# Kernel tuning notes

Hardware: AMD Instinct MI355X
Metric: run time of the kernel (lower is better)

## Reference

```python
import jax, jax.numpy as jnp
import numpy as np

B, T, N_EMBED, HEAD_SIZE = 512, 256, 384, 64

def setup_inputs() -> dict:
    key = jax.random.key(0)
    k1, k2, k3, k4 = jax.random.split(key, 4)
    x = jax.random.normal(k1, (B, T, N_EMBED), dtype=jnp.float32)
    # nn.Linear(n_embed, head_size, bias=False) weights, stored as [in, out] for x @ W
    scale = 1.0 / np.sqrt(N_EMBED)
    Wk = jax.random.uniform(k2, (N_EMBED, HEAD_SIZE), jnp.float32, -scale, scale)
    Wq = jax.random.uniform(k3, (N_EMBED, HEAD_SIZE), jnp.float32, -scale, scale)
    Wv = jax.random.uniform(k4, (N_EMBED, HEAD_SIZE), jnp.float32, -scale, scale)
    return {"x": x, "Wk": Wk, "Wq": Wq, "Wv": Wv}

def reference(x, Wk, Wq, Wv):
    # Single causal self-attention head (dropout in eval mode / identity)
    k = x @ Wk  # [B, T, H]
    q = x @ Wq
    v = x @ Wv
    wei = jnp.einsum('bth,bsh->bts', q, k) * (HEAD_SIZE ** -0.5)  # [B, T, T]
    causal = jnp.tril(jnp.ones((T, T), dtype=bool))
    wei = jnp.where(causal, wei, -jnp.inf)
    wei = jax.nn.softmax(wei, axis=-1)
    out = jnp.einsum('bts,bsh->bth', wei, v)  # [B, T, H]
    return out
```

## Files before the change

### kernel.cpp

```cpp
#include <hip/hip_runtime.h>
#include <stdint.h>


typedef short s16x8 __attribute__((ext_vector_type(8)));
typedef short s16x4 __attribute__((ext_vector_type(4)));
typedef float f32x4 __attribute__((ext_vector_type(4)));

#define LOG2E_OVER_8 0.18033688011112042f

__device__ inline short f2bf(float f) {
  union { float f; uint32_t u; } v; v.f = f;
  uint32_t r = (v.u + 0x7fffu + ((v.u >> 16) & 1u)) >> 16;
  return (short)r;
}

__global__ __launch_bounds__(256) void prep_w(const float* __restrict__ Wk,
                                              const float* __restrict__ Wq,
                                              const float* __restrict__ Wv,
                                              short* __restrict__ Wt3) {
  int idx = blockIdx.x * 256 + threadIdx.x;
  int j = idx & 7;
  int lane = (idx >> 3) & 63;
  int rest = idx >> 9;
  int ntile = rest % 12;
  int kc = rest / 12;
  int n = ntile * 16 + (lane & 15);
  int kk = (lane >> 4) * 8 + j;
  int col = n & 63;
  int w = n >> 6;
  const float* W = (w == 0) ? Wk : (w == 1) ? Wq : Wv;
  float v = W[(kc * 32 + kk) * 64 + col];
  if (w == 1) v *= LOG2E_OVER_8;
  Wt3[idx] = f2bf(v);
}

__global__ __launch_bounds__(1024) void fused_head(const float* __restrict__ x,
                                                   const short* __restrict__ Wt3,
                                                   float* __restrict__ out) {
  __shared__ __align__(16) short LDS[81920];
  short* Kf = LDS;
  short* Qf = LDS + 16384;
  short* Vf = LDS + 32768;
  short* Pb = LDS + 49152;
  short* Xc = LDS + 49152;
  short* Wsl = LDS + 49152 + 8192;

  const int tid = threadIdx.x;
  const int wave = tid >> 6;
  const int lane = tid & 63;
  const int l15 = lane & 15;
  const int quad = lane >> 4;
  const int b = blockIdx.x;
  const float* xb = x + (long)b * (256 * 384);

  const int mgrp = wave >> 2;
  const int ngrp = wave & 3;

  const int m0s = tid >> 3;
  const int kq0 = (tid & 7) * 4;
  const int xoff0 = m0s * 384 + kq0;
  const int xoff1 = xoff0 + 128 * 384;
  const int lds0 = (m0s >> 4) * 512 + ((m0s & 15) + (kq0 >> 3) * 16) * 8 + (kq0 & 7);
  const int lds1 = lds0 + 8 * 512;
  const bool wact = (tid < 768);

  f32x4 acc[4][3];
#pragma unroll
  for (int i = 0; i < 4; ++i)
#pragma unroll
    for (int k2 = 0; k2 < 3; ++k2) acc[i][k2] = (f32x4)0.0f;

  f32x4 xa0 = *(const f32x4*)(xb + xoff0);
  f32x4 xa1 = *(const f32x4*)(xb + xoff1);
  s16x8 wv;
  if (wact) wv = *(const s16x8*)(Wt3 + tid * 8);

  for (int kc = 0; kc < 12; ++kc) {
    __syncthreads();
    s16x4 h0, h1;
    h0[0] = f2bf(xa0[0]); h0[1] = f2bf(xa0[1]); h0[2] = f2bf(xa0[2]); h0[3] = f2bf(xa0[3]);
    h1[0] = f2bf(xa1[0]); h1[1] = f2bf(xa1[1]); h1[2] = f2bf(xa1[2]); h1[3] = f2bf(xa1[3]);
    *(s16x4*)(Xc + lds0) = h0;
    *(s16x4*)(Xc + lds1) = h1;
    if (wact) *(s16x8*)(Wsl + tid * 8) = wv;
    __syncthreads();
    if (kc < 11) {
      xa0 = *(const f32x4*)(xb + xoff0 + (kc + 1) * 32);
      xa1 = *(const f32x4*)(xb + xoff1 + (kc + 1) * 32);
      if (wact) wv = *(const s16x8*)(Wt3 + (kc + 1) * 6144 + tid * 8);
    }
    s16x8 af[4];
#pragma unroll
    for (int i = 0; i < 4; ++i)
      af[i] = *(const s16x8*)(Xc + (mgrp * 4 + i) * 512 + lane * 8);
#pragma unroll
    for (int k2 = 0; k2 < 3; ++k2) {
      s16x8 bfv = *(const s16x8*)(Wsl + (ngrp * 3 + k2) * 512 + lane * 8);
#pragma unroll
      for (int i = 0; i < 4; ++i)
        acc[i][k2] = __builtin_amdgcn_mfma_f32_16x16x32_bf16(af[i], bfv, acc[i][k2], 0, 0, 0);
    }
  }

#pragma unroll
  for (int i = 0; i < 4; ++i) {
    const int rowb = (mgrp * 4 + i) * 16 + quad * 4;
#pragma unroll
    for (int k2 = 0; k2 < 3; ++k2) {
      const int nt = ngrp * 3 + k2;
      const int h = (nt * 16 + l15) & 63;
      const int which = nt >> 2;
#pragma unroll
      for (int r = 0; r < 4; ++r) {
        const short v = f2bf(acc[i][k2][r]);
        const int row = rowb + r;
        if (which == 0)
          Kf[((row >> 4) * 2 + (h >> 5)) * 512 + ((row & 15) + ((h & 31) >> 3) * 16) * 8 + (h & 7)] = v;
        else if (which == 1)
          Qf[((row >> 4) * 2 + (h >> 5)) * 512 + ((row & 15) + ((h & 31) >> 3) * 16) * 8 + (h & 7)] = v;
        else
          Vf[((row >> 5) * 4 + (h >> 4)) * 512 + ((h & 15) + ((row & 31) >> 3) * 16) * 8 + (row & 7)] = v;
      }
    }
  }
  __syncthreads();

  const int t = wave;
  const int q0 = t * 16;
  short* Pw = Pb + wave * 2048;

  s16x8 qf0 = *(const s16x8*)(Qf + (t * 2 + 0) * 512 + lane * 8);
  s16x8 qf1 = *(const s16x8*)(Qf + (t * 2 + 1) * 512 + lane * 8);

  f32x4 Oacc[4];
#pragma unroll
  for (int n = 0; n < 4; ++n) Oacc[n] = (f32x4)0.0f;
  float mrow[4] = {-1e30f, -1e30f, -1e30f, -1e30f};
  float lrow[4] = {0.f, 0.f, 0.f, 0.f};

  const int nb = (t >= 8) ? 2 : 1;
  for (int cb = 0; cb < nb; ++cb) {
    const int st0 = cb * 8;
    const bool last = (cb == nb - 1);
    const int nuse = last ? (t - cb * 8 + 1) : 8;

    float S[8][4];
#pragma unroll
    for (int n = 0; n < 8; ++n) {
      if (n < nuse) {
        s16x8 kf0 = *(const s16x8*)(Kf + ((st0 + n) * 2 + 0) * 512 + lane * 8);
        s16x8 kf1 = *(const s16x8*)(Kf + ((st0 + n) * 2 + 1) * 512 + lane * 8);
        f32x4 z = (f32x4)0.0f;
        z = __builtin_amdgcn_mfma_f32_16x16x32_bf16(qf0, kf0, z, 0, 0, 0);
        z = __builtin_amdgcn_mfma_f32_16x16x32_bf16(qf1, kf1, z, 0, 0, 0);
        if (last) {
          const int s_abs = cb * 128 + n * 16 + l15;
#pragma unroll
          for (int r = 0; r < 4; ++r) {
            const int q_abs = q0 + quad * 4 + r;
            S[n][r] = (s_abs > q_abs) ? -1e30f : z[r];
          }
        } else {
#pragma unroll
          for (int r = 0; r < 4; ++r) S[n][r] = z[r];
        }
      } else {
#pragma unroll
        for (int r = 0; r < 4; ++r) S[n][r] = -1e30f;
      }
    }

    float alpha[4];
#pragma unroll
    for (int r = 0; r < 4; ++r) {
      float mx = S[0][r];
#pragma unroll
      for (int n = 1; n < 8; ++n) mx = fmaxf(mx, S[n][r]);
      mx = fmaxf(mx, __shfl_xor(mx, 1));
      mx = fmaxf(mx, __shfl_xor(mx, 2));
      mx = fmaxf(mx, __shfl_xor(mx, 4));
      mx = fmaxf(mx, __shfl_xor(mx, 8));
      float mnew = fmaxf(mrow[r], mx);
      alpha[r] = __builtin_amdgcn_exp2f(mrow[r] - mnew);
      mrow[r] = mnew;
    }
    float rs[4] = {0.f, 0.f, 0.f, 0.f};
#pragma unroll
    for (int n = 0; n < 8; ++n) {
#pragma unroll
      for (int r = 0; r < 4; ++r) {
        float p = __builtin_amdgcn_exp2f(S[n][r] - mrow[r]);
        rs[r] += p;
        Pw[(n >> 1) * 512 + ((quad * 4 + r) + ((n & 1) * 2 + (l15 >> 3)) * 16) * 8 + (l15 & 7)] = f2bf(p);
      }
    }
#pragma unroll
    for (int r = 0; r < 4; ++r) {
      float s = rs[r];
      s += __shfl_xor(s, 1);
      s += __shfl_xor(s, 2);
      s += __shfl_xor(s, 4);
      s += __shfl_xor(s, 8);
      lrow[r] = lrow[r] * alpha[r] + s;
#pragma unroll
      for (int n = 0; n < 4; ++n) Oacc[n][r] *= alpha[r];
    }
    asm volatile("s_waitcnt lgkmcnt(0)" ::: "memory");

    const int kblks = (nuse + 1) >> 1;
    for (int sb = 0; sb < kblks; ++sb) {
      s16x8 pf = *(const s16x8*)(Pw + sb * 512 + lane * 8);
#pragma unroll
      for (int n2 = 0; n2 < 4; ++n2) {
        s16x8 vfv = *(const s16x8*)(Vf + ((cb * 4 + sb) * 4 + n2) * 512 + lane * 8);
        Oacc[n2] = __builtin_amdgcn_mfma_f32_16x16x32_bf16(pf, vfv, Oacc[n2], 0, 0, 0);
      }
    }
  }

  float inv[4];
#pragma unroll
  for (int r = 0; r < 4; ++r) inv[r] = 1.0f / lrow[r];
  float* ob = out + ((long)b * 256 + q0 + quad * 4) * 64;
#pragma unroll
  for (int n = 0; n < 4; ++n)
#pragma unroll
    for (int r = 0; r < 4; ++r)
      ob[r * 64 + n * 16 + l15] = Oacc[n][r] * inv[r];
}

extern "C" void kernel_launch(void* const* d_in, const int* in_sizes, int n_in,
                              void* d_out, int out_size, void* d_ws, size_t ws_size,
                              hipStream_t stream) {
  const float* x = (const float*)d_in[0];
  const float* Wk = (const float*)d_in[1];
  const float* Wq = (const float*)d_in[2];
  const float* Wv = (const float*)d_in[3];
  float* out = (float*)d_out;
  short* Wt3 = (short*)d_ws;

  prep_w<<<288, 256, 0, stream>>>(Wk, Wq, Wv, Wt3);
  fused_head<<<512, 1024, 0, stream>>>(x, Wt3, out);
}
```

Baseline: 317.2 us.

## Fold weight prep into fused kernel and double-buffer the projection LDS stage

Removes the separate prep_w launch. Each block now loads the fp32 Wk/Wq/Wv values itself, scales Q by log2e/8, and converts them to bf16 inside the projection loop. The X/W staging area in LDS becomes two alternating buffers, which removes one __syncthreads per k-chunk, and x is prefetched two chunks ahead. The cost is redundant weight conversion in every block, done with strided scalar global loads, plus more live registers from the extra prefetch.

```diff
diff --git a/kernel.cpp b/kernel.cpp
--- a/kernel.cpp
+++ b/kernel.cpp
@@ -14,36 +14,16 @@
   return (short)r;
 }
 
-__global__ __launch_bounds__(256) void prep_w(const float* __restrict__ Wk,
-                                              const float* __restrict__ Wq,
-                                              const float* __restrict__ Wv,
-                                              short* __restrict__ Wt3) {
-  int idx = blockIdx.x * 256 + threadIdx.x;
-  int j = idx & 7;
-  int lane = (idx >> 3) & 63;
-  int rest = idx >> 9;
-  int ntile = rest % 12;
-  int kc = rest / 12;
-  int n = ntile * 16 + (lane & 15);
-  int kk = (lane >> 4) * 8 + j;
-  int col = n & 63;
-  int w = n >> 6;
-  const float* W = (w == 0) ? Wk : (w == 1) ? Wq : Wv;
-  float v = W[(kc * 32 + kk) * 64 + col];
-  if (w == 1) v *= LOG2E_OVER_8;
-  Wt3[idx] = f2bf(v);
-}
-
 __global__ __launch_bounds__(1024) void fused_head(const float* __restrict__ x,
-                                                   const short* __restrict__ Wt3,
+                                                   const float* __restrict__ Wk,
+                                                   const float* __restrict__ Wq,
+                                                   const float* __restrict__ Wv,
                                                    float* __restrict__ out) {
   __shared__ __align__(16) short LDS[81920];
   short* Kf = LDS;
   short* Qf = LDS + 16384;
   short* Vf = LDS + 32768;
   short* Pb = LDS + 49152;
-  short* Xc = LDS + 49152;
-  short* Wsl = LDS + 49152 + 8192;
 
   const int tid = threadIdx.x;
   const int wave = tid >> 6;
@@ -64,38 +44,74 @@
   const int lds1 = lds0 + 8 * 512;
   const bool wact = (tid < 768);
 
+  const int wntile = tid >> 6;
+  const int wn = wntile * 16 + l15;
+  const int wcol = wn & 63;
+  const int ww = wn >> 6;
+  const float* Wsel = (ww == 0) ? Wk : (ww == 1) ? Wq : Wv;
+  const float wscale = (ww == 1) ? LOG2E_OVER_8 : 1.0f;
+  const int wbase = (lane >> 4) * 8 * 64 + wcol;
+
   f32x4 acc[4][3];
 #pragma unroll
   for (int i = 0; i < 4; ++i)
 #pragma unroll
     for (int k2 = 0; k2 < 3; ++k2) acc[i][k2] = (f32x4)0.0f;
 
-  f32x4 xa0 = *(const f32x4*)(xb + xoff0);
-  f32x4 xa1 = *(const f32x4*)(xb + xoff1);
-  s16x8 wv;
-  if (wact) wv = *(const s16x8*)(Wt3 + tid * 8);
-
+  f32x4 xA0 = *(const f32x4*)(xb + xoff0);
+  f32x4 xA1 = *(const f32x4*)(xb + xoff1);
+  f32x4 xB0 = *(const f32x4*)(xb + xoff0 + 32);
+  f32x4 xB1 = *(const f32x4*)(xb + xoff1 + 32);
+  float wf[8];
+  if (wact) {
+#pragma unroll
+    for (int j = 0; j < 8; ++j) wf[j] = Wsel[wbase + j * 64];
+  }
+
+#pragma unroll
   for (int kc = 0; kc < 12; ++kc) {
+    short* XcS = LDS + 49152 + (kc & 1) * 14336;
+    short* WslS = XcS + 8192;
+
+    {
+      const f32x4 cx0 = (kc & 1) ? xB0 : xA0;
+      const f32x4 cx1 = (kc & 1) ? xB1 : xA1;
+      s16x4 h0, h1;
+      h0[0] = f2bf(cx0[0]); h0[1] = f2bf(cx0[1]); h0[2] = f2bf(cx0[2]); h0[3] = f2bf(cx0[3]);
+      h1[0] = f2bf(cx1[0]); h1[1] = f2bf(cx1[1]); h1[2] = f2bf(cx1[2]); h1[3] = f2bf(cx1[3]);
+      *(s16x4*)(XcS + lds0) = h0;
+      *(s16x4*)(XcS + lds1) = h1;
+    }
+    if (wact) {
+      s16x8 wv8;
+#pragma unroll
+      for (int j = 0; j < 8; ++j) wv8[j] = f2bf(wf[j] * wscale);
+      *(s16x8*)(WslS + tid * 8) = wv8;
+    }
+
     __syncthreads();
-    s16x4 h0, h1;
-    h0[0] = f2bf(xa0[0]); h0[1] = f2bf(xa0[1]); h0[2] = f2bf(xa0[2]); h0[3] = f2bf(xa0[3]);
-    h1[0] = f2bf(xa1[0]); h1[1] = f2bf(xa1[1]); h1[2] = f2bf(xa1[2]); h1[3] = f2bf(xa1[3]);
-    *(s16x4*)(Xc + lds0) = h0;
-    *(s16x4*)(Xc + lds1) = h1;
-    if (wact) *(s16x8*)(Wsl + tid * 8) = wv;
-    __syncthreads();
-    if (kc < 11) {
-      xa0 = *(const f32x4*)(xb + xoff0 + (kc + 1) * 32);
-      xa1 = *(const f32x4*)(xb + xoff1 + (kc + 1) * 32);
-      if (wact) wv = *(const s16x8*)(Wt3 + (kc + 1) * 6144 + tid * 8);
-    }
+
+    if (kc + 2 < 12) {
+      if (kc & 1) {
+        xB0 = *(const f32x4*)(xb + xoff0 + (kc + 2) * 32);
+        xB1 = *(const f32x4*)(xb + xoff1 + (kc + 2) * 32);
+      } else {
+        xA0 = *(const f32x4*)(xb + xoff0 + (kc + 2) * 32);
+        xA1 = *(const f32x4*)(xb + xoff1 + (kc + 2) * 32);
+      }
+    }
+    if (wact && (kc + 1 < 12)) {
+#pragma unroll
+      for (int j = 0; j < 8; ++j) wf[j] = Wsel[(kc + 1) * 2048 + wbase + j * 64];
+    }
+
     s16x8 af[4];
 #pragma unroll
     for (int i = 0; i < 4; ++i)
-      af[i] = *(const s16x8*)(Xc + (mgrp * 4 + i) * 512 + lane * 8);
+      af[i] = *(const s16x8*)(XcS + (mgrp * 4 + i) * 512 + lane * 8);
 #pragma unroll
     for (int k2 = 0; k2 < 3; ++k2) {
-      s16x8 bfv = *(const s16x8*)(Wsl + (ngrp * 3 + k2) * 512 + lane * 8);
+      s16x8 bfv = *(const s16x8*)(WslS + (ngrp * 3 + k2) * 512 + lane * 8);
 #pragma unroll
       for (int i = 0; i < 4; ++i)
         acc[i][k2] = __builtin_amdgcn_mfma_f32_16x16x32_bf16(af[i], bfv, acc[i][k2], 0, 0, 0);
@@ -237,8 +253,6 @@
   const float* Wq = (const float*)d_in[2];
   const float* Wv = (const float*)d_in[3];
   float* out = (float*)d_out;
-  short* Wt3 = (short*)d_ws;
-
-  prep_w<<<288, 256, 0, stream>>>(Wk, Wq, Wv, Wt3);
-  fused_head<<<512, 1024, 0, stream>>>(x, Wt3, out);
+  (void)d_ws; (void)ws_size;
+  fused_head<<<512, 1024, 0, stream>>>(x, Wk, Wq, Wv, out);
 }
```

Result: slower. 325.2 us (+2.5%).

## Double-buffer projection LDS tiles and prefetch x two chunks ahead

Applied to the files above, without the earlier changes.

The QKV projection loop now alternates between two LDS buffers for the bf16 x chunk and weight slice. This removes one of the two __syncthreads per k-chunk. x loads are issued two chunks ahead in alternating register sets, and the loop is fully unrolled. The launch bounds also gain a minimum-occupancy hint, which may cap register allocation and cause spills. The extra buffer uses more LDS, though the total still fits in the existing shared array.

```diff
diff --git a/kernel.cpp b/kernel.cpp
--- a/kernel.cpp
+++ b/kernel.cpp
@@ -34,16 +34,14 @@
   Wt3[idx] = f2bf(v);
 }
 
-__global__ __launch_bounds__(1024) void fused_head(const float* __restrict__ x,
-                                                   const short* __restrict__ Wt3,
-                                                   float* __restrict__ out) {
+__global__ __launch_bounds__(1024, 4) void fused_head(const float* __restrict__ x,
+                                                      const short* __restrict__ Wt3,
+                                                      float* __restrict__ out) {
   __shared__ __align__(16) short LDS[81920];
   short* Kf = LDS;
   short* Qf = LDS + 16384;
   short* Vf = LDS + 32768;
   short* Pb = LDS + 49152;
-  short* Xc = LDS + 49152;
-  short* Wsl = LDS + 49152 + 8192;
 
   const int tid = threadIdx.x;
   const int wave = tid >> 6;
@@ -70,32 +68,50 @@
 #pragma unroll
     for (int k2 = 0; k2 < 3; ++k2) acc[i][k2] = (f32x4)0.0f;
 
-  f32x4 xa0 = *(const f32x4*)(xb + xoff0);
-  f32x4 xa1 = *(const f32x4*)(xb + xoff1);
+  f32x4 xA0 = *(const f32x4*)(xb + xoff0);
+  f32x4 xA1 = *(const f32x4*)(xb + xoff1);
+  f32x4 xB0 = *(const f32x4*)(xb + xoff0 + 32);
+  f32x4 xB1 = *(const f32x4*)(xb + xoff1 + 32);
   s16x8 wv;
   if (wact) wv = *(const s16x8*)(Wt3 + tid * 8);
 
+#pragma unroll
   for (int kc = 0; kc < 12; ++kc) {
+    short* XcS = LDS + 49152 + (kc & 1) * 14336;
+    short* WslS = XcS + 8192;
+
+    {
+      const f32x4 cx0 = (kc & 1) ? xB0 : xA0;
+      const f32x4 cx1 = (kc & 1) ? xB1 : xA1;
+      s16x4 h0, h1;
+      h0[0] = f2bf(cx0[0]); h0[1] = f2bf(cx0[1]); h0[2] = f2bf(cx0[2]); h0[3] = f2bf(cx0[3]);
+      h1[0] = f2bf(cx1[0]); h1[1] = f2bf(cx1[1]); h1[2] = f2bf(cx1[2]); h1[3] = f2bf(cx1[3]);
+      *(s16x4*)(XcS + lds0) = h0;
+      *(s16x4*)(XcS + lds1) = h1;
+    }
+    if (wact) *(s16x8*)(WslS + tid * 8) = wv;
+
     __syncthreads();
-    s16x4 h0, h1;
-    h0[0] = f2bf(xa0[0]); h0[1] = f2bf(xa0[1]); h0[2] = f2bf(xa0[2]); h0[3] = f2bf(xa0[3]);
-    h1[0] = f2bf(xa1[0]); h1[1] = f2bf(xa1[1]); h1[2] = f2bf(xa1[2]); h1[3] = f2bf(xa1[3]);
-    *(s16x4*)(Xc + lds0) = h0;
-    *(s16x4*)(Xc + lds1) = h1;
-    if (wact) *(s16x8*)(Wsl + tid * 8) = wv;
-    __syncthreads();
-    if (kc < 11) {
-      xa0 = *(const f32x4*)(xb + xoff0 + (kc + 1) * 32);
-      xa1 = *(const f32x4*)(xb + xoff1 + (kc + 1) * 32);
-      if (wact) wv = *(const s16x8*)(Wt3 + (kc + 1) * 6144 + tid * 8);
-    }
+
+    if (kc + 2 < 12) {
+      if (kc & 1) {
+        xB0 = *(const f32x4*)(xb + xoff0 + (kc + 2) * 32);
+        xB1 = *(const f32x4*)(xb + xoff1 + (kc + 2) * 32);
+      } else {
+        xA0 = *(const f32x4*)(xb + xoff0 + (kc + 2) * 32);
+        xA1 = *(const f32x4*)(xb + xoff1 + (kc + 2) * 32);
+      }
+    }
+    if (wact && (kc + 1 < 12))
+      wv = *(const s16x8*)(Wt3 + (kc + 1) * 6144 + tid * 8);
+
     s16x8 af[4];
 #pragma unroll
     for (int i = 0; i < 4; ++i)
-      af[i] = *(const s16x8*)(Xc + (mgrp * 4 + i) * 512 + lane * 8);
+      af[i] = *(const s16x8*)(XcS + (mgrp * 4 + i) * 512 + lane * 8);
 #pragma unroll
     for (int k2 = 0; k2 < 3; ++k2) {
-      s16x8 bfv = *(const s16x8*)(Wsl + (ngrp * 3 + k2) * 512 + lane * 8);
+      s16x8 bfv = *(const s16x8*)(WslS + (ngrp * 3 + k2) * 512 + lane * 8);
 #pragma unroll
       for (int i = 0; i < 4; ++i)
         acc[i][k2] = __builtin_amdgcn_mfma_f32_16x16x32_bf16(af[i], bfv, acc[i][k2], 0, 0, 0);
```

After: 317.6 us. No clear change (+0.1%).

## Split fused head kernel into separate projection and attention kernels with smaller blocks

Applied to the files above, without the earlier changes.

Replaces the single 1024-thread fused kernel with two 256-thread kernels: a projection kernel that writes K/Q/V in bf16 fragment layout to a global workspace, and an attention kernel that reads K/V directly from global memory. Each block now handles a quarter of a batch's query tiles, which raises block count and occupancy and cuts the large LDS footprint. The cost is an extra global round-trip for K/Q/V, an extra launch, and attention blocks redundantly reading the same K/V from global/L2 instead of LDS.

```diff
diff --git a/kernel.cpp b/kernel.cpp
--- a/kernel.cpp
+++ b/kernel.cpp
@@ -3,7 +3,6 @@
 
 
 typedef short s16x8 __attribute__((ext_vector_type(8)));
-typedef short s16x4 __attribute__((ext_vector_type(4)));
 typedef float f32x4 __attribute__((ext_vector_type(4)));
 
 #define LOG2E_OVER_8 0.18033688011112042f
@@ -34,103 +33,117 @@
   Wt3[idx] = f2bf(v);
 }
 
-__global__ __launch_bounds__(1024) void fused_head(const float* __restrict__ x,
-                                                   const short* __restrict__ Wt3,
-                                                   float* __restrict__ out) {
-  __shared__ __align__(16) short LDS[81920];
-  short* Kf = LDS;
-  short* Qf = LDS + 16384;
-  short* Vf = LDS + 32768;
-  short* Pb = LDS + 49152;
-  short* Xc = LDS + 49152;
-  short* Wsl = LDS + 49152 + 8192;
+__global__ __launch_bounds__(256, 4) void proj(const float* __restrict__ x,
+                                               const short* __restrict__ Wt3,
+                                               short* __restrict__ kqv) {
+  __shared__ __align__(16) short Wl[12288];
 
   const int tid = threadIdx.x;
   const int wave = tid >> 6;
   const int lane = tid & 63;
   const int l15 = lane & 15;
   const int quad = lane >> 4;
-  const int b = blockIdx.x;
-  const float* xb = x + (long)b * (256 * 384);
-
-  const int mgrp = wave >> 2;
-  const int ngrp = wave & 3;
-
-  const int m0s = tid >> 3;
-  const int kq0 = (tid & 7) * 4;
-  const int xoff0 = m0s * 384 + kq0;
-  const int xoff1 = xoff0 + 128 * 384;
-  const int lds0 = (m0s >> 4) * 512 + ((m0s & 15) + (kq0 >> 3) * 16) * 8 + (kq0 & 7);
-  const int lds1 = lds0 + 8 * 512;
-  const bool wact = (tid < 768);
-
-  f32x4 acc[4][3];
-#pragma unroll
-  for (int i = 0; i < 4; ++i)
-#pragma unroll
-    for (int k2 = 0; k2 < 3; ++k2) acc[i][k2] = (f32x4)0.0f;
-
-  f32x4 xa0 = *(const f32x4*)(xb + xoff0);
-  f32x4 xa1 = *(const f32x4*)(xb + xoff1);
-  s16x8 wv;
-  if (wact) wv = *(const s16x8*)(Wt3 + tid * 8);
-
+  const int blk = blockIdx.x;
+  const int b = blk >> 2;
+  const int tb = (blk & 3) * 4;
+  const int t = tb + wave;
+
+  const float* xw = x + (long)b * (256 * 384) + (t * 16 + l15) * 384 + quad * 8;
+  const int so = tid * 8;
+
+  f32x4 acc[12];
+#pragma unroll
+  for (int nt = 0; nt < 12; ++nt) acc[nt] = (f32x4)0.0f;
+
+  f32x4 xa0 = *(const f32x4*)(xw);
+  f32x4 xa1 = *(const f32x4*)(xw + 4);
+  s16x8 w0 = *(const s16x8*)(Wt3 + so);
+  s16x8 w1 = *(const s16x8*)(Wt3 + so + 2048);
+  s16x8 w2 = *(const s16x8*)(Wt3 + so + 4096);
+
+#pragma unroll
   for (int kc = 0; kc < 12; ++kc) {
+    short* buf = Wl + (kc & 1) * 6144;
+    *(s16x8*)(buf + so) = w0;
+    *(s16x8*)(buf + so + 2048) = w1;
+    *(s16x8*)(buf + so + 4096) = w2;
+
+    s16x8 af;
+    af[0] = f2bf(xa0[0]); af[1] = f2bf(xa0[1]); af[2] = f2bf(xa0[2]); af[3] = f2bf(xa0[3]);
+    af[4] = f2bf(xa1[0]); af[5] = f2bf(xa1[1]); af[6] = f2bf(xa1[2]); af[7] = f2bf(xa1[3]);
+
     __syncthreads();
-    s16x4 h0, h1;
-    h0[0] = f2bf(xa0[0]); h0[1] = f2bf(xa0[1]); h0[2] = f2bf(xa0[2]); h0[3] = f2bf(xa0[3]);
-    h1[0] = f2bf(xa1[0]); h1[1] = f2bf(xa1[1]); h1[2] = f2bf(xa1[2]); h1[3] = f2bf(xa1[3]);
-    *(s16x4*)(Xc + lds0) = h0;
-    *(s16x4*)(Xc + lds1) = h1;
-    if (wact) *(s16x8*)(Wsl + tid * 8) = wv;
-    __syncthreads();
+
     if (kc < 11) {
-      xa0 = *(const f32x4*)(xb + xoff0 + (kc + 1) * 32);
-      xa1 = *(const f32x4*)(xb + xoff1 + (kc + 1) * 32);
-      if (wact) wv = *(const s16x8*)(Wt3 + (kc + 1) * 6144 + tid * 8);
-    }
-    s16x8 af[4];
-#pragma unroll
-    for (int i = 0; i < 4; ++i)
-      af[i] = *(const s16x8*)(Xc + (mgrp * 4 + i) * 512 + lane * 8);
-#pragma unroll
-    for (int k2 = 0; k2 < 3; ++k2) {
-      s16x8 bfv = *(const s16x8*)(Wsl + (ngrp * 3 + k2) * 512 + lane * 8);
-#pragma unroll
-      for (int i = 0; i < 4; ++i)
-        acc[i][k2] = __builtin_amdgcn_mfma_f32_16x16x32_bf16(af[i], bfv, acc[i][k2], 0, 0, 0);
-    }
-  }
-
-#pragma unroll
-  for (int i = 0; i < 4; ++i) {
-    const int rowb = (mgrp * 4 + i) * 16 + quad * 4;
-#pragma unroll
-    for (int k2 = 0; k2 < 3; ++k2) {
-      const int nt = ngrp * 3 + k2;
-      const int h = (nt * 16 + l15) & 63;
-      const int which = nt >> 2;
-#pragma unroll
-      for (int r = 0; r < 4; ++r) {
-        const short v = f2bf(acc[i][k2][r]);
-        const int row = rowb + r;
-        if (which == 0)
-          Kf[((row >> 4) * 2 + (h >> 5)) * 512 + ((row & 15) + ((h & 31) >> 3) * 16) * 8 + (h & 7)] = v;
-        else if (which == 1)
-          Qf[((row >> 4) * 2 + (h >> 5)) * 512 + ((row & 15) + ((h & 31) >> 3) * 16) * 8 + (h & 7)] = v;
-        else
-          Vf[((row >> 5) * 4 + (h >> 4)) * 512 + ((h & 15) + ((row & 31) >> 3) * 16) * 8 + (row & 7)] = v;
-      }
+      xa0 = *(const f32x4*)(xw + (kc + 1) * 32);
+      xa1 = *(const f32x4*)(xw + (kc + 1) * 32 + 4);
+      w0 = *(const s16x8*)(Wt3 + (kc + 1) * 6144 + so);
+      w1 = *(const s16x8*)(Wt3 + (kc + 1) * 6144 + so + 2048);
+      w2 = *(const s16x8*)(Wt3 + (kc + 1) * 6144 + so + 4096);
+    }
+
+#pragma unroll
+    for (int nt = 0; nt < 12; ++nt) {
+      s16x8 bfv = *(const s16x8*)(buf + nt * 512 + lane * 8);
+      acc[nt] = __builtin_amdgcn_mfma_f32_16x16x32_bf16(af, bfv, acc[nt], 0, 0, 0);
     }
   }
   __syncthreads();
 
-  const int t = wave;
+  const int base_sub = tb * 1024;
+#pragma unroll
+  for (int nt = 0; nt < 12; ++nt) {
+    const int h = (nt * 16 + l15) & 63;
+    const int which = nt >> 2;
+#pragma unroll
+    for (int r = 0; r < 4; ++r) {
+      const short v = f2bf(acc[nt][r]);
+      const int row = t * 16 + quad * 4 + r;
+      if (which == 2) {
+        const int idx = ((row >> 5) * 4 + (h >> 4)) * 512 +
+                        ((h & 15) + ((row & 31) >> 3) * 16) * 8 + (row & 7) - base_sub;
+        Wl[8192 + idx] = v;
+      } else {
+        const int idx = ((row >> 4) * 2 + (h >> 5)) * 512 +
+                        ((row & 15) + ((h & 31) >> 3) * 16) * 8 + (h & 7) - base_sub;
+        Wl[which * 4096 + idx] = v;
+      }
+    }
+  }
+  __syncthreads();
+
+  short* dstK = kqv + (long)b * 49152 + base_sub;
+  short* dstQ = dstK + 16384;
+  short* dstV = dstK + 32768;
+  *(s16x8*)(dstK + so)        = *(const s16x8*)(Wl + so);
+  *(s16x8*)(dstK + 2048 + so) = *(const s16x8*)(Wl + 2048 + so);
+  *(s16x8*)(dstQ + so)        = *(const s16x8*)(Wl + 4096 + so);
+  *(s16x8*)(dstQ + 2048 + so) = *(const s16x8*)(Wl + 6144 + so);
+  *(s16x8*)(dstV + so)        = *(const s16x8*)(Wl + 8192 + so);
+  *(s16x8*)(dstV + 2048 + so) = *(const s16x8*)(Wl + 10240 + so);
+}
+
+__global__ __launch_bounds__(256, 4) void attn(const short* __restrict__ kqv,
+                                               float* __restrict__ out) {
+  __shared__ __align__(16) short P[8192];
+
+  const int tid = threadIdx.x;
+  const int wave = tid >> 6;
+  const int lane = tid & 63;
+  const int l15 = lane & 15;
+  const int quad = lane >> 4;
+  const int blk = blockIdx.x;
+  const int b = blk >> 2;
+  const int t = (blk & 3) * 4 + wave;
   const int q0 = t * 16;
-  short* Pw = Pb + wave * 2048;
-
-  s16x8 qf0 = *(const s16x8*)(Qf + (t * 2 + 0) * 512 + lane * 8);
-  s16x8 qf1 = *(const s16x8*)(Qf + (t * 2 + 1) * 512 + lane * 8);
+
+  const short* Kg = kqv + (long)b * 49152;
+  const short* Qg = Kg + 16384;
+  const short* Vg = Kg + 32768;
+  short* Pw = P + wave * 2048;
+
+  s16x8 qf0 = *(const s16x8*)(Qg + (t * 2 + 0) * 512 + lane * 8);
+  s16x8 qf1 = *(const s16x8*)(Qg + (t * 2 + 1) * 512 + lane * 8);
 
   f32x4 Oacc[4];
 #pragma unroll
@@ -148,8 +161,8 @@
 #pragma unroll
     for (int n = 0; n < 8; ++n) {
       if (n < nuse) {
-        s16x8 kf0 = *(const s16x8*)(Kf + ((st0 + n) * 2 + 0) * 512 + lane * 8);
-        s16x8 kf1 = *(const s16x8*)(Kf + ((st0 + n) * 2 + 1) * 512 + lane * 8);
+        s16x8 kf0 = *(const s16x8*)(Kg + ((st0 + n) * 2 + 0) * 512 + lane * 8);
+        s16x8 kf1 = *(const s16x8*)(Kg + ((st0 + n) * 2 + 1) * 512 + lane * 8);
         f32x4 z = (f32x4)0.0f;
         z = __builtin_amdgcn_mfma_f32_16x16x32_bf16(qf0, kf0, z, 0, 0, 0);
         z = __builtin_amdgcn_mfma_f32_16x16x32_bf16(qf1, kf1, z, 0, 0, 0);
@@ -212,7 +225,7 @@
       s16x8 pf = *(const s16x8*)(Pw + sb * 512 + lane * 8);
 #pragma unroll
       for (int n2 = 0; n2 < 4; ++n2) {
-        s16x8 vfv = *(const s16x8*)(Vf + ((cb * 4 + sb) * 4 + n2) * 512 + lane * 8);
+        s16x8 vfv = *(const s16x8*)(Vg + ((cb * 4 + sb) * 4 + n2) * 512 + lane * 8);
         Oacc[n2] = __builtin_amdgcn_mfma_f32_16x16x32_bf16(pf, vfv, Oacc[n2], 0, 0, 0);
       }
     }
@@ -238,7 +251,9 @@
   const float* Wv = (const float*)d_in[3];
   float* out = (float*)d_out;
   short* Wt3 = (short*)d_ws;
+  short* kqv = (short*)d_ws + (1 << 20) / 2;
 
   prep_w<<<288, 256, 0, stream>>>(Wk, Wq, Wv, Wt3);
-  fused_head<<<512, 1024, 0, stream>>>(x, Wt3, out);
-}
+  proj<<<2048, 256, 0, stream>>>(x, Wt3, kqv);
+  attn<<<2048, 256, 0, stream>>>(kqv, out);
+}
```

Result: slower. 341.7 us (+7.7%).
